# Performance work log

Measured on AMD Instinct MI355X. Metric: run time of the kernel, lower is better.

The kernel has to match this reference:

```python
import jax, jax.numpy as jnp
import numpy as np
from jax import lax

D_MODEL = 1024
D_STATE = 16
D_CONV = 4
EXPAND = 2
D_INNER = EXPAND * D_MODEL          # 2048
DT_RANK = (D_MODEL + 15) // 16      # 64
FF_INNER = 4 * D_MODEL              # 4096
B, L = 2, 2048
EPS = 1e-5


def _layer_norm(x, g, b):
    mu = jnp.mean(x, axis=-1, keepdims=True)
    var = jnp.mean(jnp.square(x - mu), axis=-1, keepdims=True)
    return (x - mu) * lax.rsqrt(var + EPS) * g + b


def setup_inputs() -> dict:
    key = jax.random.key(0)
    ks = jax.random.split(key, 10)
    def n(k, shape, s=0.02):
        return jax.random.normal(k, shape, dtype=jnp.float32) * s
    x = jax.random.normal(ks[0], (B, L, D_MODEL), dtype=jnp.float32)
    return dict(
        x=x,
        ln1_g=jnp.ones((D_MODEL,), jnp.float32), ln1_b=jnp.zeros((D_MODEL,), jnp.float32),
        w_in=n(ks[1], (D_MODEL, 2 * D_INNER)),
        conv_w=n(ks[2], (D_INNER, D_CONV), 0.2), conv_b=jnp.zeros((D_INNER,), jnp.float32),
        w_x=n(ks[3], (D_INNER, DT_RANK + 2 * D_STATE)),
        w_dt=n(ks[4], (DT_RANK, D_INNER), 0.1),
        b_dt=jnp.full((D_INNER,), -4.6, jnp.float32),  # softplus(-4.6) ~= 0.01 dt init
        a_log=jnp.log(jnp.broadcast_to(jnp.arange(1, D_STATE + 1, dtype=jnp.float32), (D_INNER, D_STATE))),
        d_skip=jnp.ones((D_INNER,), jnp.float32),
        w_out=n(ks[5], (D_INNER, D_MODEL)),
        ln2_g=jnp.ones((D_MODEL,), jnp.float32), ln2_b=jnp.zeros((D_MODEL,), jnp.float32),
        w_ff1=n(ks[6], (D_MODEL, 2 * FF_INNER)), b_ff1=jnp.zeros((2 * FF_INNER,), jnp.float32),
        w_ff2=n(ks[7], (FF_INNER, D_MODEL)), b_ff2=jnp.zeros((D_MODEL,), jnp.float32),
    )


def _mamba(h, w_in, conv_w, conv_b, w_x, w_dt, b_dt, a_log, d_skip, w_out):
    # h: (B, L, D_MODEL)
    xz = h @ w_in                                   # (B, L, 2*D_INNER)
    xc, z = jnp.split(xz, 2, axis=-1)               # each (B, L, D_INNER)
    # depthwise causal conv1d along L
    xc_t = jnp.transpose(xc, (0, 2, 1))             # (B, D_INNER, L)
    xc_t = lax.conv_general_dilated(
        xc_t, conv_w[:, None, :], window_strides=(1,), padding=[(D_CONV - 1, 0)],
        feature_group_count=D_INNER, dimension_numbers=('NCH', 'OIH', 'NCH'))
    xc = jnp.transpose(xc_t, (0, 2, 1)) + conv_b
    xc = jax.nn.silu(xc)
    # input-dependent dt, B, C
    dbc = xc @ w_x                                  # (B, L, DT_RANK+2*D_STATE)
    dt_lo, Bm, Cm = jnp.split(dbc, [DT_RANK, DT_RANK + D_STATE], axis=-1)
    dt = jax.nn.softplus(dt_lo @ w_dt + b_dt)       # (B, L, D_INNER)
    A = -jnp.exp(a_log)                             # (D_INNER, D_STATE)

    def step(hst, inp):
        dt_t, B_t, C_t, x_t = inp                   # (B,di),(B,N),(B,N),(B,di)
        dA = jnp.exp(dt_t[..., None] * A)           # (B, D_INNER, D_STATE)
        hst = hst * dA + (dt_t * x_t)[..., None] * B_t[:, None, :]
        y = jnp.einsum('bdn,bn->bd', hst, C_t)
        return hst, y

    h0 = jnp.zeros((h.shape[0], D_INNER, D_STATE), dt.dtype)
    xs = (jnp.swapaxes(dt, 0, 1), jnp.swapaxes(Bm, 0, 1),
          jnp.swapaxes(Cm, 0, 1), jnp.swapaxes(xc, 0, 1))
    _, ys = lax.scan(step, h0, xs)                  # ys: (L, B, D_INNER)
    y = jnp.swapaxes(ys, 0, 1) + d_skip * xc
    y = y * jax.nn.silu(z)
    return y @ w_out                                # (B, L, D_MODEL)


def _geglu_ff(h, w1, b1, w2, b2):
    p = h @ w1 + b1
    a, g = jnp.split(p, 2, axis=-1)
    return (a * jax.nn.gelu(g)) @ w2 + b2


def reference(x, ln1_g, ln1_b, w_in, conv_w, conv_b, w_x, w_dt, b_dt, a_log,
              d_skip, w_out, ln2_g, ln2_b, w_ff1, b_ff1, w_ff2, b_ff2):
    h = _layer_norm(x, ln1_g, ln1_b)
    x = x + _mamba(h, w_in, conv_w, conv_b, w_x, w_dt, b_dt, a_log, d_skip, w_out)
    h2 = _layer_norm(x, ln2_g, ln2_b)
    x = x + _geglu_ff(h2, w_ff1, b_ff1, w_ff2, b_ff2)
    return x
```

## Files before the change

### kernel.cpp

```cpp
#include <hip/hip_runtime.h>
#include <hip/hip_bf16.h>
#include <stdint.h>
#include <stddef.h>


typedef __bf16 bf16;
typedef __bf16 bf16x8 __attribute__((ext_vector_type(8)));
typedef float  f32x4  __attribute__((ext_vector_type(4)));

static constexpr int kB  = 2;
static constexpr int kL  = 2048;
static constexpr int kDM = 1024;
static constexpr int kDI = 2048;
static constexpr int kM  = kB * kL;
static constexpr int kNC = 16;
static constexpr int kCH = kL / kNC;

__device__ __forceinline__ void gload16(const void* g, void* l) {
  __builtin_amdgcn_global_load_lds((__attribute__((address_space(1))) void*)g,
                                   (__attribute__((address_space(3))) void*)l,
                                   16, 0, 0);
}

__global__ __launch_bounds__(256) void transpose_to_bf16(
    const float* __restrict__ w, bf16* __restrict__ wt, int K, int N, int Npad) {
  __shared__ float t[32][33];
  const int k0 = blockIdx.x * 32, n0 = blockIdx.y * 32;
  const int tx = threadIdx.x & 31, ty = threadIdx.x >> 5;
#pragma unroll
  for (int i = ty; i < 32; i += 8) {
    float v = 0.f;
    if (k0 + i < K && n0 + tx < N) v = w[(size_t)(k0 + i) * N + n0 + tx];
    t[i][tx] = v;
  }
  __syncthreads();
#pragma unroll
  for (int i = ty; i < 32; i += 8) {
    const int n = n0 + i, k = k0 + tx;
    if (n < Npad && k < K) wt[(size_t)n * K + k] = (bf16)t[tx][i];
  }
}

__global__ __launch_bounds__(256) void layernorm_to_bf16(
    const float* __restrict__ x, const float* __restrict__ g,
    const float* __restrict__ b, bf16* __restrict__ out) {
  const int row = blockIdx.x;
  const float4 v = ((const float4*)(x + (size_t)row * kDM))[threadIdx.x];
  float s  = v.x + v.y + v.z + v.w;
  float s2 = v.x * v.x + v.y * v.y + v.z * v.z + v.w * v.w;
#pragma unroll
  for (int off = 1; off < 64; off <<= 1) {
    s  += __shfl_xor(s, off);
    s2 += __shfl_xor(s2, off);
  }
  __shared__ float ws[4], ws2[4];
  const int wave = threadIdx.x >> 6, lane = threadIdx.x & 63;
  if (lane == 0) { ws[wave] = s; ws2[wave] = s2; }
  __syncthreads();
  s  = ws[0] + ws[1] + ws[2] + ws[3];
  s2 = ws2[0] + ws2[1] + ws2[2] + ws2[3];
  const float mu  = s * (1.f / kDM);
  const float var = s2 * (1.f / kDM) - mu * mu;
  const float r   = rsqrtf(var + 1e-5f);
  const int c = threadIdx.x * 4;
  const float4 gg = ((const float4*)g)[threadIdx.x];
  const float4 bb = ((const float4*)b)[threadIdx.x];
  bf16* o = out + (size_t)row * kDM + c;
  o[0] = (bf16)((v.x - mu) * r * gg.x + bb.x);
  o[1] = (bf16)((v.y - mu) * r * gg.y + bb.y);
  o[2] = (bf16)((v.z - mu) * r * gg.z + bb.z);
  o[3] = (bf16)((v.w - mu) * r * gg.w + bb.w);
}

template <int MODE>
__global__ __launch_bounds__(256, 2) void gemm_bt(
    const bf16* __restrict__ A, int lda,
    const bf16* __restrict__ BT, int ldbt, int K,
    float* __restrict__ C0, bf16* __restrict__ C1,
    const float* __restrict__ bias, const float* __restrict__ res) {
  __shared__ __align__(16) bf16 As[128 * 32];
  __shared__ __align__(16) bf16 Bs[128 * 32];

  const int tid  = threadIdx.x;
  const int wave = tid >> 6;
  const int lane = tid & 63;
  const int m0 = blockIdx.y * 128;
  const int n0 = blockIdx.x * 128;
  const int wr = wave >> 1, wc = wave & 1;
  const int lr = lane & 15, kg = lane >> 4;

  const int srow = lane >> 2;
  const int scol = (lane & 3) * 8;

  const bf16* Ag0 = A  + (size_t)(m0 + wave * 32 + srow) * lda  + scol;
  const bf16* Ag1 = Ag0 + (size_t)16 * lda;
  const bf16* Bg0 = BT + (size_t)(n0 + wave * 32 + srow) * ldbt + scol;
  const bf16* Bg1 = Bg0 + (size_t)16 * ldbt;
  bf16* Al0 = As + wave * 1024;
  bf16* Al1 = Al0 + 512;
  bf16* Bl0 = Bs + wave * 1024;
  bf16* Bl1 = Bl0 + 512;

  f32x4 acc[4][4] = {};

  for (int kt = 0; kt < K; kt += 32) {
    __syncthreads();
    gload16(Ag0 + kt, Al0);
    gload16(Ag1 + kt, Al1);
    gload16(Bg0 + kt, Bl0);
    gload16(Bg1 + kt, Bl1);
    __syncthreads();

    bf16x8 af[4], bfr[4];
#pragma unroll
    for (int i = 0; i < 4; ++i) {
      af[i]  = *(const bf16x8*)(As + (wr * 64 + i * 16 + lr) * 32 + kg * 8);
      bfr[i] = *(const bf16x8*)(Bs + (wc * 64 + i * 16 + lr) * 32 + kg * 8);
    }
#pragma unroll
    for (int i = 0; i < 4; ++i)
#pragma unroll
      for (int j = 0; j < 4; ++j)
        acc[i][j] =
            __builtin_amdgcn_mfma_f32_16x16x32_bf16(af[i], bfr[j], acc[i][j], 0, 0, 0);
  }

#pragma unroll
  for (int i = 0; i < 4; ++i) {
    const int mbase = m0 + wr * 64 + i * 16 + kg * 4;
#pragma unroll
    for (int j = 0; j < 4; ++j) {
      const int n = n0 + wc * 64 + j * 16 + lr;
#pragma unroll
      for (int e = 0; e < 4; ++e) {
        const int m = mbase + e;
        const float v = acc[i][j][e];
        if constexpr (MODE == 0) {
          if (n < kDI) C0[(size_t)m * kDI + n] = v;
          else         C1[(size_t)m * kDI + (n - kDI)] = (bf16)(v / (1.f + expf(-v)));
        } else if constexpr (MODE == 1) {
          C0[(size_t)m * 128 + n] = v;
          if (n < 64) C1[(size_t)m * 64 + n] = (bf16)v;
        } else if constexpr (MODE == 2) {
          const float t = v + bias[n];
          const float sp = (t > 0.f) ? (t + log1pf(expf(-t))) : log1pf(expf(t));
          C0[(size_t)m * kDI + n] = sp;
        } else if constexpr (MODE == 3) {
          C0[(size_t)m * kDM + n] = v + res[(size_t)m * kDM + n];
        } else if constexpr (MODE == 4) {
          C1[(size_t)m * 8192 + n] = (bf16)(v + bias[n]);
        } else {
          C0[(size_t)m * kDM + n] = v + bias[n] + res[(size_t)m * kDM + n];
        }
      }
    }
  }
}

__global__ __launch_bounds__(256) void conv_silu(
    const float* __restrict__ xc_raw, const float* __restrict__ cw,
    const float* __restrict__ cb, float* __restrict__ xf, bf16* __restrict__ xb) {
  const int idx = blockIdx.x * 256 + threadIdx.x;
  const int d = idx & (kDI - 1);
  const int m = idx >> 11;
  const int l = m & (kL - 1);
  float acc = cb[d];
  const float w0 = cw[d * 4 + 0], w1 = cw[d * 4 + 1], w2 = cw[d * 4 + 2],
              w3 = cw[d * 4 + 3];
  if (l >= 3) acc += xc_raw[(size_t)(m - 3) * kDI + d] * w0;
  if (l >= 2) acc += xc_raw[(size_t)(m - 2) * kDI + d] * w1;
  if (l >= 1) acc += xc_raw[(size_t)(m - 1) * kDI + d] * w2;
  acc += xc_raw[(size_t)m * kDI + d] * w3;
  const float a = acc / (1.f + expf(-acc));
  xf[idx] = a;
  xb[idx] = (bf16)a;
}


__global__ __launch_bounds__(256) void scan_p1(
    const float* __restrict__ dt, const float* __restrict__ xc,
    const float* __restrict__ dbc, const float* __restrict__ a_log,
    float* __restrict__ P, float* __restrict__ Q) {
  const int c  = blockIdx.x & 15;
  const int dg = (blockIdx.x >> 4) & 127;
  const int b  = blockIdx.x >> 11;
  const int dl = threadIdx.x >> 4, n = threadIdx.x & 15;
  const int d  = dg * 16 + dl;
  const float Adn = -expf(a_log[d * 16 + n]);
  const size_t rb = ((size_t)b * kL + c * kCH) * kDI + d;
  const size_t qb = ((size_t)b * kL + c * kCH) * 128 + 64 + n;
  float h = 0.f, sdt = 0.f;
#pragma unroll 8
  for (int l = 0; l < kCH; ++l) {
    const float dtv = dt[rb + (size_t)l * kDI];
    const float xv  = xc[rb + (size_t)l * kDI];
    const float Bv  = dbc[qb + (size_t)l * 128];
    const float dA  = __expf(dtv * Adn);
    h = h * dA + dtv * xv * Bv;
    sdt += dtv;
  }
  const int idx = ((b * kNC + c) * kDI + d) * 16 + n;
  P[idx] = __expf(sdt * Adn);
  Q[idx] = h;
}

__global__ __launch_bounds__(256) void scan_p2(
    const float* __restrict__ P, const float* __restrict__ Q,
    float* __restrict__ H0) {
  const int i  = blockIdx.x * 256 + threadIdx.x;
  const int dn = i & (kDI * 16 - 1);
  const int b  = i >> 15;
  float h = 0.f;
#pragma unroll
  for (int c = 0; c < kNC; ++c) {
    const int idx = (b * kNC + c) * (kDI * 16) + dn;
    H0[idx] = h;
    h = P[idx] * h + Q[idx];
  }
}

__global__ __launch_bounds__(256) void scan_p3(
    const float* __restrict__ dt, const float* __restrict__ xc,
    const float* __restrict__ dbc, const float* __restrict__ a_log,
    const float* __restrict__ d_skip, const bf16* __restrict__ zs,
    const float* __restrict__ H0, bf16* __restrict__ y) {
  const int c  = blockIdx.x & 15;
  const int dg = (blockIdx.x >> 4) & 127;
  const int b  = blockIdx.x >> 11;
  const int dl = threadIdx.x >> 4, n = threadIdx.x & 15;
  const int d  = dg * 16 + dl;
  const float Adn = -expf(a_log[d * 16 + n]);
  const float dsk = d_skip[d];
  const size_t rb = ((size_t)b * kL + c * kCH) * kDI + d;
  const size_t qb = ((size_t)b * kL + c * kCH) * 128;
  float h = H0[((b * kNC + c) * kDI + d) * 16 + n];
#pragma unroll 4
  for (int l = 0; l < kCH; ++l) {
    const size_t r = rb + (size_t)l * kDI;
    const size_t q = qb + (size_t)l * 128;
    const float dtv = dt[r];
    const float xv  = xc[r];
    const float Bv  = dbc[q + 64 + n];
    const float Cv  = dbc[q + 80 + n];
    const float dA  = __expf(dtv * Adn);
    h = h * dA + dtv * xv * Bv;
    float part = h * Cv;
    part += __shfl_xor(part, 1);
    part += __shfl_xor(part, 2);
    part += __shfl_xor(part, 4);
    part += __shfl_xor(part, 8);
    if (n == 0) {
      y[r] = (bf16)((part + dsk * xv) * (float)zs[r]);
    }
  }
}

__global__ __launch_bounds__(256) void geglu(
    const bf16* __restrict__ p, bf16* __restrict__ v) {
  const int idx = blockIdx.x * 256 + threadIdx.x;
  const int m = idx >> 12, n = idx & 4095;
  const float a = (float)p[(size_t)m * 8192 + n];
  const float g = (float)p[(size_t)m * 8192 + 4096 + n];
  const float g3 = g * g * g;
  const float t  = tanhf(0.7978845608028654f * (g + 0.044715f * g3));
  v[idx] = (bf16)(a * (0.5f * g * (1.f + t)));
}

extern "C" void kernel_launch(void* const* d_in, const int* in_sizes, int n_in,
                              void* d_out, int out_size, void* d_ws, size_t ws_size,
                              hipStream_t stream) {
  const float* x      = (const float*)d_in[0];
  const float* ln1_g  = (const float*)d_in[1];
  const float* ln1_b  = (const float*)d_in[2];
  const float* w_in   = (const float*)d_in[3];
  const float* conv_w = (const float*)d_in[4];
  const float* conv_b = (const float*)d_in[5];
  const float* w_x    = (const float*)d_in[6];
  const float* w_dt   = (const float*)d_in[7];
  const float* b_dt   = (const float*)d_in[8];
  const float* a_log  = (const float*)d_in[9];
  const float* d_skip = (const float*)d_in[10];
  const float* w_out  = (const float*)d_in[11];
  const float* ln2_g  = (const float*)d_in[12];
  const float* ln2_b  = (const float*)d_in[13];
  const float* w_ff1  = (const float*)d_in[14];
  const float* b_ff1  = (const float*)d_in[15];
  const float* w_ff2  = (const float*)d_in[16];
  const float* b_ff2  = (const float*)d_in[17];
  float* out = (float*)d_out;
  char* ws = (char*)d_ws;

  bf16* wT_in  = (bf16*)(ws + 0);
  bf16* wT_x   = (bf16*)(ws + 8388608);
  bf16* wT_dt  = (bf16*)(ws + 8912896);
  bf16* wT_out = (bf16*)(ws + 9175040);
  bf16* wT_ff1 = (bf16*)(ws + 13369344);
  bf16* wT_ff2 = (bf16*)(ws + 30146560);
  bf16* h_bf   = (bf16*)(ws + 38535168);
  float* xcraw = (float*)(ws + 46923776);
  bf16* zs     = (bf16*)(ws + 80478208);
  float* xcf   = (float*)(ws + 97255424);
  bf16* xcb    = (bf16*)(ws + 130809856);
  float* dbc   = (float*)(ws + 147587072);
  bf16* dtlo   = (bf16*)(ws + 149684224);
  bf16* pbuf   = (bf16*)(ws + 150208512);
  float* dtbuf = xcraw;
  bf16*  vbuf  = (bf16*)xcraw;
  float* out1  = (float*)zs;
  bf16*  ybuf  = xcb;
  bf16*  h2    = h_bf;
  float* Pbuf  = (float*)pbuf;
  float* Qbuf  = (float*)((char*)pbuf + (4 << 20));
  float* H0buf = (float*)((char*)pbuf + (8 << 20));

  const dim3 tb(256);
  transpose_to_bf16<<<dim3(32, 128), tb, 0, stream>>>(w_in, wT_in, 1024, 4096, 4096);
  transpose_to_bf16<<<dim3(64, 4), tb, 0, stream>>>(w_x, wT_x, 2048, 96, 128);
  transpose_to_bf16<<<dim3(2, 64), tb, 0, stream>>>(w_dt, wT_dt, 64, 2048, 2048);
  transpose_to_bf16<<<dim3(64, 32), tb, 0, stream>>>(w_out, wT_out, 2048, 1024, 1024);
  transpose_to_bf16<<<dim3(32, 256), tb, 0, stream>>>(w_ff1, wT_ff1, 1024, 8192, 8192);
  transpose_to_bf16<<<dim3(128, 32), tb, 0, stream>>>(w_ff2, wT_ff2, 4096, 1024, 1024);

  layernorm_to_bf16<<<kM, tb, 0, stream>>>(x, ln1_g, ln1_b, h_bf);

  gemm_bt<0><<<dim3(32, 32), tb, 0, stream>>>(h_bf, 1024, wT_in, 1024, 1024,
                                              xcraw, zs, nullptr, nullptr);
  conv_silu<<<(kM * kDI) / 256, tb, 0, stream>>>(xcraw, conv_w, conv_b, xcf, xcb);

  gemm_bt<1><<<dim3(1, 32), tb, 0, stream>>>(xcb, 2048, wT_x, 2048, 2048,
                                             dbc, dtlo, nullptr, nullptr);
  gemm_bt<2><<<dim3(16, 32), tb, 0, stream>>>(dtlo, 64, wT_dt, 64, 64,
                                              dtbuf, nullptr, b_dt, nullptr);

  scan_p1<<<kB * 128 * kNC, tb, 0, stream>>>(dtbuf, xcf, dbc, a_log, Pbuf, Qbuf);
  scan_p2<<<(kB * kDI * 16) / 256, tb, 0, stream>>>(Pbuf, Qbuf, H0buf);
  scan_p3<<<kB * 128 * kNC, tb, 0, stream>>>(dtbuf, xcf, dbc, a_log, d_skip,
                                             zs, H0buf, ybuf);

  gemm_bt<3><<<dim3(8, 32), tb, 0, stream>>>(ybuf, 2048, wT_out, 2048, 2048,
                                             out1, nullptr, nullptr, x);
  layernorm_to_bf16<<<kM, tb, 0, stream>>>(out1, ln2_g, ln2_b, h2);

  gemm_bt<4><<<dim3(64, 32), tb, 0, stream>>>(h2, 1024, wT_ff1, 1024, 1024,
                                              nullptr, pbuf, b_ff1, nullptr);
  geglu<<<(kM * 4096) / 256, tb, 0, stream>>>(pbuf, vbuf);

  gemm_bt<5><<<dim3(8, 32), tb, 0, stream>>>(vbuf, 4096, wT_ff2, 4096, 4096,
                                             out, nullptr, b_ff2, out1);
  (void)in_sizes; (void)n_in; (void)out_size; (void)ws_size;
}
```

Baseline: 833.0 us.

## Restructure selective scan to one channel per thread with shared-memory B/C and more chunks

The chunked selective scan now gives each thread one channel with all 16 state values held in registers, instead of spreading the 16 states across 16 lanes. Per-timestep B and C vectors are staged once per block in shared memory and read back as vector loads. The chunk count rises from 16 to 64 so the grid keeps enough parallelism despite fewer threads per channel. This removes the cross-lane shuffle reduction and the 16x redundant dt/x loads per channel, at the cost of more registers per thread, larger P/Q/H0 buffers and a longer sequential pass over chunks in scan_p2.

Result: faster. 687.9 us (-17.4%).

```diff
diff --git a/kernel.cpp b/kernel.cpp
--- a/kernel.cpp
+++ b/kernel.cpp
@@ -13,7 +13,7 @@
 static constexpr int kDM = 1024;
 static constexpr int kDI = 2048;
 static constexpr int kM  = kB * kL;
-static constexpr int kNC = 16;
+static constexpr int kNC = 64;
 static constexpr int kCH = kL / kNC;
 
 __device__ __forceinline__ void gload16(const void* g, void* l) {
@@ -181,27 +181,56 @@
     const float* __restrict__ dt, const float* __restrict__ xc,
     const float* __restrict__ dbc, const float* __restrict__ a_log,
     float* __restrict__ P, float* __restrict__ Q) {
-  const int c  = blockIdx.x & 15;
-  const int dg = (blockIdx.x >> 4) & 127;
-  const int b  = blockIdx.x >> 11;
-  const int dl = threadIdx.x >> 4, n = threadIdx.x & 15;
-  const int d  = dg * 16 + dl;
-  const float Adn = -expf(a_log[d * 16 + n]);
+  const int dg = blockIdx.x & 7;
+  const int c  = (blockIdx.x >> 3) & (kNC - 1);
+  const int b  = blockIdx.x >> 9;
+  const int d  = dg * 256 + threadIdx.x;
+  __shared__ __align__(16) float BC[kCH][32];
+  {
+    const int l  = threadIdx.x >> 3;
+    const int cg = (threadIdx.x & 7) * 4;
+    *(float4*)&BC[l][cg] =
+        *(const float4*)&dbc[(size_t)(b * kL + c * kCH + l) * 128 + 64 + cg];
+  }
+  __syncthreads();
+  float A[16];
+#pragma unroll
+  for (int q = 0; q < 4; ++q) {
+    const float4 al = *(const float4*)&a_log[d * 16 + q * 4];
+    A[q * 4 + 0] = -__expf(al.x);
+    A[q * 4 + 1] = -__expf(al.y);
+    A[q * 4 + 2] = -__expf(al.z);
+    A[q * 4 + 3] = -__expf(al.w);
+  }
+  float h[16] = {};
+  float sdt = 0.f;
   const size_t rb = ((size_t)b * kL + c * kCH) * kDI + d;
-  const size_t qb = ((size_t)b * kL + c * kCH) * 128 + 64 + n;
-  float h = 0.f, sdt = 0.f;
-#pragma unroll 8
+#pragma unroll 2
   for (int l = 0; l < kCH; ++l) {
     const float dtv = dt[rb + (size_t)l * kDI];
     const float xv  = xc[rb + (size_t)l * kDI];
-    const float Bv  = dbc[qb + (size_t)l * 128];
-    const float dA  = __expf(dtv * Adn);
-    h = h * dA + dtv * xv * Bv;
+    const float u   = dtv * xv;
     sdt += dtv;
-  }
-  const int idx = ((b * kNC + c) * kDI + d) * 16 + n;
-  P[idx] = __expf(sdt * Adn);
-  Q[idx] = h;
+    float Bv[16];
+    *(float4*)&Bv[0]  = *(const float4*)&BC[l][0];
+    *(float4*)&Bv[4]  = *(const float4*)&BC[l][4];
+    *(float4*)&Bv[8]  = *(const float4*)&BC[l][8];
+    *(float4*)&Bv[12] = *(const float4*)&BC[l][12];
+#pragma unroll
+    for (int n = 0; n < 16; ++n) {
+      const float dA = __expf(dtv * A[n]);
+      h[n] = h[n] * dA + u * Bv[n];
+    }
+  }
+  const size_t o = (((size_t)b * kNC + c) * kDI + d) * 16;
+  float Pv[16];
+#pragma unroll
+  for (int n = 0; n < 16; ++n) Pv[n] = __expf(sdt * A[n]);
+#pragma unroll
+  for (int q = 0; q < 4; ++q) {
+    *(float4*)&P[o + q * 4] = *(float4*)&Pv[q * 4];
+    *(float4*)&Q[o + q * 4] = *(float4*)&h[q * 4];
+  }
 }
 
 __global__ __launch_bounds__(256) void scan_p2(
@@ -211,9 +240,9 @@
   const int dn = i & (kDI * 16 - 1);
   const int b  = i >> 15;
   float h = 0.f;
-#pragma unroll
+#pragma unroll 8
   for (int c = 0; c < kNC; ++c) {
-    const int idx = (b * kNC + c) * (kDI * 16) + dn;
+    const size_t idx = ((size_t)(b * kNC + c)) * (kDI * 16) + dn;
     H0[idx] = h;
     h = P[idx] * h + Q[idx];
   }
@@ -224,34 +253,59 @@
     const float* __restrict__ dbc, const float* __restrict__ a_log,
     const float* __restrict__ d_skip, const bf16* __restrict__ zs,
     const float* __restrict__ H0, bf16* __restrict__ y) {
-  const int c  = blockIdx.x & 15;
-  const int dg = (blockIdx.x >> 4) & 127;
-  const int b  = blockIdx.x >> 11;
-  const int dl = threadIdx.x >> 4, n = threadIdx.x & 15;
-  const int d  = dg * 16 + dl;
-  const float Adn = -expf(a_log[d * 16 + n]);
+  const int dg = blockIdx.x & 7;
+  const int c  = (blockIdx.x >> 3) & (kNC - 1);
+  const int b  = blockIdx.x >> 9;
+  const int d  = dg * 256 + threadIdx.x;
+  __shared__ __align__(16) float BC[kCH][32];
+  {
+    const int l  = threadIdx.x >> 3;
+    const int cg = (threadIdx.x & 7) * 4;
+    *(float4*)&BC[l][cg] =
+        *(const float4*)&dbc[(size_t)(b * kL + c * kCH + l) * 128 + 64 + cg];
+  }
+  __syncthreads();
+  float A[16];
+#pragma unroll
+  for (int q = 0; q < 4; ++q) {
+    const float4 al = *(const float4*)&a_log[d * 16 + q * 4];
+    A[q * 4 + 0] = -__expf(al.x);
+    A[q * 4 + 1] = -__expf(al.y);
+    A[q * 4 + 2] = -__expf(al.z);
+    A[q * 4 + 3] = -__expf(al.w);
+  }
   const float dsk = d_skip[d];
+  float h[16];
+  const size_t o = (((size_t)b * kNC + c) * kDI + d) * 16;
+#pragma unroll
+  for (int q = 0; q < 4; ++q)
+    *(float4*)&h[q * 4] = *(const float4*)&H0[o + q * 4];
   const size_t rb = ((size_t)b * kL + c * kCH) * kDI + d;
-  const size_t qb = ((size_t)b * kL + c * kCH) * 128;
-  float h = H0[((b * kNC + c) * kDI + d) * 16 + n];
-#pragma unroll 4
+#pragma unroll 2
   for (int l = 0; l < kCH; ++l) {
-    const size_t r = rb + (size_t)l * kDI;
-    const size_t q = qb + (size_t)l * 128;
+    const size_t r  = rb + (size_t)l * kDI;
     const float dtv = dt[r];
     const float xv  = xc[r];
-    const float Bv  = dbc[q + 64 + n];
-    const float Cv  = dbc[q + 80 + n];
-    const float dA  = __expf(dtv * Adn);
-    h = h * dA + dtv * xv * Bv;
-    float part = h * Cv;
-    part += __shfl_xor(part, 1);
-    part += __shfl_xor(part, 2);
-    part += __shfl_xor(part, 4);
-    part += __shfl_xor(part, 8);
-    if (n == 0) {
-      y[r] = (bf16)((part + dsk * xv) * (float)zs[r]);
+    const float zv  = (float)zs[r];
+    const float u   = dtv * xv;
+    float Bv[16], Cv[16];
+    *(float4*)&Bv[0]  = *(const float4*)&BC[l][0];
+    *(float4*)&Bv[4]  = *(const float4*)&BC[l][4];
+    *(float4*)&Bv[8]  = *(const float4*)&BC[l][8];
+    *(float4*)&Bv[12] = *(const float4*)&BC[l][12];
+    *(float4*)&Cv[0]  = *(const float4*)&BC[l][16];
+    *(float4*)&Cv[4]  = *(const float4*)&BC[l][20];
+    *(float4*)&Cv[8]  = *(const float4*)&BC[l][24];
+    *(float4*)&Cv[12] = *(const float4*)&BC[l][28];
+    float pp[4] = {0.f, 0.f, 0.f, 0.f};
+#pragma unroll
+    for (int n = 0; n < 16; ++n) {
+      const float dA = __expf(dtv * A[n]);
+      h[n] = h[n] * dA + u * Bv[n];
+      pp[n & 3] += h[n] * Cv[n];
     }
+    const float part = (pp[0] + pp[1]) + (pp[2] + pp[3]);
+    y[r] = (bf16)((part + dsk * xv) * zv);
   }
 }
 
@@ -310,8 +364,8 @@
   bf16*  ybuf  = xcb;
   bf16*  h2    = h_bf;
   float* Pbuf  = (float*)pbuf;
-  float* Qbuf  = (float*)((char*)pbuf + (4 << 20));
-  float* H0buf = (float*)((char*)pbuf + (8 << 20));
+  float* Qbuf  = (float*)((char*)pbuf + (16 << 20));
+  float* H0buf = (float*)((char*)pbuf + (32 << 20));
 
   const dim3 tb(256);
   transpose_to_bf16<<<dim3(32, 128), tb, 0, stream>>>(w_in, wT_in, 1024, 4096, 4096);
@@ -332,10 +386,11 @@
   gemm_bt<2><<<dim3(16, 32), tb, 0, stream>>>(dtlo, 64, wT_dt, 64, 64,
                                               dtbuf, nullptr, b_dt, nullptr);
 
-  scan_p1<<<kB * 128 * kNC, tb, 0, stream>>>(dtbuf, xcf, dbc, a_log, Pbuf, Qbuf);
+  scan_p1<<<kB * kNC * (kDI / 256), tb, 0, stream>>>(dtbuf, xcf, dbc, a_log,
+                                                     Pbuf, Qbuf);
   scan_p2<<<(kB * kDI * 16) / 256, tb, 0, stream>>>(Pbuf, Qbuf, H0buf);
-  scan_p3<<<kB * 128 * kNC, tb, 0, stream>>>(dtbuf, xcf, dbc, a_log, d_skip,
-                                             zs, H0buf, ybuf);
+  scan_p3<<<kB * kNC * (kDI / 256), tb, 0, stream>>>(dtbuf, xcf, dbc, a_log,
+                                                     d_skip, zs, H0buf, ybuf);
 
   gemm_bt<3><<<dim3(8, 32), tb, 0, stream>>>(ybuf, 2048, wT_out, 2048, 2048,
                                              out1, nullptr, nullptr, x);
```
